# Kernel tuning notes

Hardware: AMD Instinct MI355X
Metric: run time of the kernel (lower is better)

## Reference

```python
import jax, jax.numpy as jnp
import numpy as np
import math

CODE_DIMS = [32, 32]
NUM_CODEBOOK = 16
FEAT_DIM = 1024
EPS = 1e-12


def rms_norm(x, eps=EPS):
    var = jnp.mean(x * x, axis=-1, keepdims=True) + eps
    return x * jax.lax.rsqrt(var)


def outer_product(y, code_dims):
    # y: [..., h, sum(code_dims)] -> [..., h, prod(code_dims)]
    splits = list(np.cumsum(code_dims)[:-1])
    mats = jnp.split(y, splits, axis=-1)
    out = mats[0]
    for m in mats[1:]:
        out = out[..., :, None] * m[..., None, :]
        out = out.reshape(*out.shape[:-2], -1)
    return out


def setup_inputs() -> dict:
    key = jax.random.key(0)
    kx, kw = jax.random.split(key)
    x = jax.random.normal(kx, (4, 2048, FEAT_DIM), dtype=jnp.float32)
    std = math.sqrt(2.0 / (FEAT_DIM + sum(CODE_DIMS)))
    weight = jax.random.normal(kw, (NUM_CODEBOOK, FEAT_DIM, sum(CODE_DIMS)), dtype=jnp.float32) * std
    return {"x": x, "weight": weight}


def reference(x, weight):
    h = weight.shape[0]
    # batched per-codebook linear: [..., d] x [h, d, o] -> [..., h, o]
    y = jnp.einsum('...i,hio->...ho', x, weight)
    # chunked outer product per codebook -> [..., h, prod(code_dims)]
    op = outer_product(y, CODE_DIMS)
    out = jnp.mean(op, axis=-2) * math.sqrt(h)
    return rms_norm(out)
```

## Files before the change

kernel.cpp:

```cpp
#include <hip/hip_runtime.h>
#include <hip/hip_bf16.h>

#define KDIM  1024
#define NOUT  1024
#define NTOK  8192
#define NCB   16
#define BM    256
#define BN    128
#define BK    64
#define TILEB 49152
#define NBUF  3

typedef __attribute__((ext_vector_type(8))) short short8;
typedef __attribute__((ext_vector_type(4))) float f32x4;

__device__ static inline unsigned short f2bf(float f) {
    unsigned int u = __float_as_uint(f);
    return (unsigned short)((u + 0x7FFFu + ((u >> 16) & 1u)) >> 16);
}

__device__ static inline float bf2f(unsigned int h) {
    return __uint_as_float(h << 16);
}

__device__ static inline void async_copy16(const void* g, void* l) {
    __builtin_amdgcn_global_load_lds(
        (const __attribute__((address_space(1))) void*)g,
        (__attribute__((address_space(3))) void*)l, 16, 0, 0);
}

__global__ __launch_bounds__(256) void conv_kernel(const float* __restrict__ x,
                                                   const float* __restrict__ W,
                                                   unsigned short* __restrict__ A,
                                                   unsigned short* __restrict__ Bt) {
    int b = blockIdx.x;
    if (b < 4096) {
        int u = b * 256 + threadIdx.x;
        const float* src = x + (size_t)u * 8;
        float4 v0 = *(const float4*)(src);
        float4 v1 = *(const float4*)(src + 4);
        short8 o;
        o[0] = (short)f2bf(v0.x); o[1] = (short)f2bf(v0.y);
        o[2] = (short)f2bf(v0.z); o[3] = (short)f2bf(v0.w);
        o[4] = (short)f2bf(v1.x); o[5] = (short)f2bf(v1.y);
        o[6] = (short)f2bf(v1.z); o[7] = (short)f2bf(v1.w);
        *(short8*)(A + (size_t)u * 8) = o;
    } else {
        int u = (b - 4096) * 256 + threadIdx.x;
        int n  = u & (NOUT - 1);
        int k0 = (u >> 10) << 3;
        int h = n >> 6, o = n & 63;
        const float* src = W + (size_t)h * KDIM * 64 + o;
        short8 v;
#pragma unroll
        for (int j = 0; j < 8; ++j)
            v[j] = (short)f2bf(src[(size_t)(k0 + j) * 64]);
        *(short8*)(Bt + (size_t)n * KDIM + k0) = v;
    }
}


template <int VM, bool STAGE>
__device__ __forceinline__ void phase0(const unsigned short* __restrict__ A,
                                       const unsigned short* __restrict__ Bt,
                                       char* lds, int tid, int m0, int n0, int kt,
                                       int wm, int wn, int r15, int q,
                                       f32x4 (&acc)[4][4]) {
    asm volatile("s_waitcnt vmcnt(%0)" :: "i"(VM) : "memory");
    __builtin_amdgcn_sched_barrier(0);
    __builtin_amdgcn_s_barrier();
    __builtin_amdgcn_sched_barrier(0);
    if (STAGE) {
        char* lb = lds + ((kt + 2) % NBUF) * TILEB;
        unsigned short* Als = (unsigned short*)lb;
        unsigned short* Bls = (unsigned short*)(lb + 32768);
        const int kel = (kt + 2) * BK;
#pragma unroll
        for (int i = 0; i < 2; ++i) {
            int s = i * 512 + tid;
            int row = s >> 3;
            int cs = (s & 7) ^ (row & 7);
            async_copy16(A + (size_t)(m0 + row) * KDIM + kel + cs * 8, Als + s * 8);
        }
        {
            int s = tid;
            int row = s >> 3;
            int cs = (s & 7) ^ (row & 7);
            async_copy16(Bt + (size_t)(n0 + row) * KDIM + kel + cs * 8, Bls + s * 8);
        }
    }
    const unsigned short* Al = (const unsigned short*)(lds + (kt % NBUF) * TILEB);
    const unsigned short* Bl = Al + 16384;
    short8 af[4], bf[4];
#pragma unroll
    for (int mf = 0; mf < 4; ++mf) {
        int row = wm * 64 + mf * 16 + r15;
        af[mf] = *(const short8*)(Al + row * 64 + ((q ^ (row & 7)) << 3));
    }
#pragma unroll
    for (int nf = 0; nf < 4; ++nf) {
        int row = wn * 64 + nf * 16 + r15;
        bf[nf] = *(const short8*)(Bl + row * 64 + ((q ^ (row & 7)) << 3));
    }
    asm volatile("s_waitcnt lgkmcnt(0)" ::: "memory");
    __builtin_amdgcn_sched_barrier(0);
    __builtin_amdgcn_s_setprio(1);
#pragma unroll
    for (int mf = 0; mf < 4; ++mf)
#pragma unroll
        for (int nf = 0; nf < 4; ++nf)
            acc[mf][nf] = __builtin_amdgcn_mfma_f32_16x16x32_bf16(af[mf], bf[nf], acc[mf][nf], 0, 0, 0);
    __builtin_amdgcn_s_setprio(0);
}

template <bool STAGE>
__device__ __forceinline__ void phase1(const unsigned short* __restrict__ A,
                                       const unsigned short* __restrict__ Bt,
                                       char* lds, int tid, int m0, int n0, int kt,
                                       int wm, int wn, int r15, int q,
                                       f32x4 (&acc)[4][4]) {
    __builtin_amdgcn_s_barrier();
    __builtin_amdgcn_sched_barrier(0);
    if (STAGE) {
        char* lb = lds + ((kt + 2) % NBUF) * TILEB;
        unsigned short* Als = (unsigned short*)lb;
        unsigned short* Bls = (unsigned short*)(lb + 32768);
        const int kel = (kt + 2) * BK;
#pragma unroll
        for (int i = 2; i < 4; ++i) {
            int s = i * 512 + tid;
            int row = s >> 3;
            int cs = (s & 7) ^ (row & 7);
            async_copy16(A + (size_t)(m0 + row) * KDIM + kel + cs * 8, Als + s * 8);
        }
        {
            int s = 512 + tid;
            int row = s >> 3;
            int cs = (s & 7) ^ (row & 7);
            async_copy16(Bt + (size_t)(n0 + row) * KDIM + kel + cs * 8, Bls + s * 8);
        }
    }
    const unsigned short* Al = (const unsigned short*)(lds + (kt % NBUF) * TILEB);
    const unsigned short* Bl = Al + 16384;
    short8 af[4], bf[4];
#pragma unroll
    for (int mf = 0; mf < 4; ++mf) {
        int row = wm * 64 + mf * 16 + r15;
        af[mf] = *(const short8*)(Al + row * 64 + (((4 + q) ^ (row & 7)) << 3));
    }
#pragma unroll
    for (int nf = 0; nf < 4; ++nf) {
        int row = wn * 64 + nf * 16 + r15;
        bf[nf] = *(const short8*)(Bl + row * 64 + (((4 + q) ^ (row & 7)) << 3));
    }
    asm volatile("s_waitcnt lgkmcnt(0)" ::: "memory");
    __builtin_amdgcn_sched_barrier(0);
    __builtin_amdgcn_s_setprio(1);
#pragma unroll
    for (int mf = 0; mf < 4; ++mf)
#pragma unroll
        for (int nf = 0; nf < 4; ++nf)
            acc[mf][nf] = __builtin_amdgcn_mfma_f32_16x16x32_bf16(af[mf], bf[nf], acc[mf][nf], 0, 0, 0);
    __builtin_amdgcn_s_setprio(0);
}

__device__ __forceinline__ void stage_full(const unsigned short* __restrict__ A,
                                           const unsigned short* __restrict__ Bt,
                                           char* lbase, int tid, int m0, int n0, int kel) {
    unsigned short* Als = (unsigned short*)lbase;
    unsigned short* Bls = (unsigned short*)(lbase + 32768);
#pragma unroll
    for (int i = 0; i < 4; ++i) {
        int s = i * 512 + tid;
        int row = s >> 3;
        int cs = (s & 7) ^ (row & 7);
        async_copy16(A + (size_t)(m0 + row) * KDIM + kel + cs * 8, Als + s * 8);
    }
#pragma unroll
    for (int i = 0; i < 2; ++i) {
        int s = i * 512 + tid;
        int row = s >> 3;
        int cs = (s & 7) ^ (row & 7);
        async_copy16(Bt + (size_t)(n0 + row) * KDIM + kel + cs * 8, Bls + s * 8);
    }
}

__global__ __launch_bounds__(512, 2) void gemm_kernel(const unsigned short* __restrict__ A,
                                                      const unsigned short* __restrict__ Bt,
                                                      unsigned short* __restrict__ Y) {
    extern __shared__ char lds[];

    const int id  = blockIdx.x;
    const int xcd = id & 7;
    const int j   = id >> 3;
    const int m0  = (xcd * 4 + (j >> 3)) * BM;
    const int n0  = (j & 7) * BN;

    const int tid  = threadIdx.x;
    const int lane = tid & 63;
    const int w    = tid >> 6;
    const int wm   = w >> 1;
    const int wn   = w & 1;
    const int r15  = lane & 15;
    const int q    = lane >> 4;

    f32x4 acc[4][4];
#pragma unroll
    for (int mf = 0; mf < 4; ++mf)
#pragma unroll
        for (int nf = 0; nf < 4; ++nf)
            acc[mf][nf] = (f32x4){0.f, 0.f, 0.f, 0.f};

    stage_full(A, Bt, lds,         tid, m0, n0, 0);
    stage_full(A, Bt, lds + TILEB, tid, m0, n0, BK);

#pragma unroll 1
    for (int kt = 0; kt < 14; ++kt) {
        phase0<6, true>(A, Bt, lds, tid, m0, n0, kt, wm, wn, r15, q, acc);
        phase1<true>   (A, Bt, lds, tid, m0, n0, kt, wm, wn, r15, q, acc);
    }
    phase0<6, false>(A, Bt, lds, tid, m0, n0, 14, wm, wn, r15, q, acc);
    phase1<false>   (A, Bt, lds, tid, m0, n0, 14, wm, wn, r15, q, acc);
    phase0<0, false>(A, Bt, lds, tid, m0, n0, 15, wm, wn, r15, q, acc);
    phase1<false>   (A, Bt, lds, tid, m0, n0, 15, wm, wn, r15, q, acc);

#pragma unroll
    for (int mf = 0; mf < 4; ++mf)
#pragma unroll
        for (int nf = 0; nf < 4; ++nf) {
            int col = n0 + wn * 64 + nf * 16 + r15;
#pragma unroll
            for (int r = 0; r < 4; ++r) {
                int row = m0 + wm * 64 + mf * 16 + q * 4 + r;
                Y[(size_t)row * NOUT + col] = f2bf(acc[mf][nf][r]);
            }
        }
}

__global__ __launch_bounds__(256) void epilogue_kernel(const unsigned short* __restrict__ Y,
                                                       float* __restrict__ out) {
    __shared__ float ylds[1024];
    __shared__ float red[4];

    const int t = blockIdx.x;
    const int tid = threadIdx.x;
    const unsigned short* yrow = Y + (size_t)t * NOUT;

    {
        uint2 raw = *(const uint2*)(yrow + tid * 4);
        ylds[tid * 4 + 0] = bf2f(raw.x & 0xffffu);
        ylds[tid * 4 + 1] = bf2f(raw.x >> 16);
        ylds[tid * 4 + 2] = bf2f(raw.y & 0xffffu);
        ylds[tid * 4 + 3] = bf2f(raw.y >> 16);
    }
    __syncthreads();

    const int jj = tid >> 3;
    const int k0 = (tid & 7) * 4;

    float o0 = 0.f, o1 = 0.f, o2 = 0.f, o3 = 0.f;
#pragma unroll
    for (int h = 0; h < NCB; ++h) {
        float a = ylds[h * 64 + jj];
        float4 bb = *(const float4*)&ylds[h * 64 + 32 + k0];
        o0 += a * bb.x; o1 += a * bb.y; o2 += a * bb.z; o3 += a * bb.w;
    }
    o0 *= 0.25f; o1 *= 0.25f; o2 *= 0.25f; o3 *= 0.25f;

    float ss = o0 * o0 + o1 * o1 + o2 * o2 + o3 * o3;
#pragma unroll
    for (int off = 32; off >= 1; off >>= 1)
        ss += __shfl_xor(ss, off, 64);

    const int lane = tid & 63, wv = tid >> 6;
    if (lane == 0) red[wv] = ss;
    __syncthreads();
    float tot = red[0] + red[1] + red[2] + red[3];
    float scale = rsqrtf(tot * (1.0f / 1024.0f) + 1e-12f);

    float4 o;
    o.x = o0 * scale; o.y = o1 * scale; o.z = o2 * scale; o.w = o3 * scale;
    *(float4*)(out + (size_t)t * 1024 + tid * 4) = o;
}

extern "C" void kernel_launch(void* const* d_in, const int* in_sizes, int n_in,
                              void* d_out, int out_size, void* d_ws, size_t ws_size,
                              hipStream_t stream) {
    const float* x   = (const float*)d_in[0];
    const float* wgt = (const float*)d_in[1];
    float* out = (float*)d_out;

    unsigned short* A  = (unsigned short*)d_ws;
    unsigned short* Bt = (unsigned short*)((char*)d_ws + (16u << 20));
    unsigned short* Y  = (unsigned short*)((char*)d_ws + (18u << 20));

    (void)hipFuncSetAttribute((const void*)gemm_kernel,
                              hipFuncAttributeMaxDynamicSharedMemorySize, NBUF * TILEB);

    conv_kernel<<<4096 + 512, 256, 0, stream>>>(x, wgt, A, Bt);
    gemm_kernel<<<(NTOK / BM) * (NOUT / BN), 512, NBUF * TILEB, stream>>>(A, Bt, Y);
    epilogue_kernel<<<NTOK, 256, 0, stream>>>(Y, out);
}
```

Baseline: 48.40 us.

## Double-buffer MFMA register fragments and remap blocks to XCDs in conv/epilogue

The GEMM main loop now prefetches the next half-tile's A/B fragments from LDS into a second register set while MFMAs run on the current set, with partial lgkmcnt waits replacing full drains. Global-to-LDS staging is split into halves, with a vmcnt wait per phase. The conversion and epilogue kernels also remap block indices so each XCD handles a contiguous range of rows. This is meant to hide LDS read latency behind matrix math and improve L2 locality, at the cost of more VGPRs and more delicate waitcnt accounting.

```diff
diff --git a/kernel.cpp b/kernel.cpp
--- a/kernel.cpp
+++ b/kernel.cpp
@@ -35,7 +35,8 @@
                                                    unsigned short* __restrict__ Bt) {
     int b = blockIdx.x;
     if (b < 4096) {
-        int u = b * 256 + threadIdx.x;
+        int bb = (b & 7) * 512 + (b >> 3);
+        int u = bb * 256 + threadIdx.x;
         const float* src = x + (size_t)u * 8;
         float4 v0 = *(const float4*)(src);
         float4 v1 = *(const float4*)(src + 4);
@@ -60,129 +61,96 @@
 }
 
 
+__device__ __forceinline__ void stage_half(const unsigned short* __restrict__ A,
+                                           const unsigned short* __restrict__ Bt,
+                                           char* lbase, int tid, int m0, int n0,
+                                           int kel, int half) {
+    unsigned short* Als = (unsigned short*)lbase;
+    unsigned short* Bls = (unsigned short*)(lbase + 32768);
+#pragma unroll
+    for (int i = 0; i < 2; ++i) {
+        int s = (half * 2 + i) * 512 + tid;
+        int row = s >> 3;
+        int cs = (s & 7) ^ (row & 7);
+        async_copy16(A + (size_t)(m0 + row) * KDIM + kel + cs * 8, Als + s * 8);
+    }
+    {
+        int s = half * 512 + tid;
+        int row = s >> 3;
+        int cs = (s & 7) ^ (row & 7);
+        async_copy16(Bt + (size_t)(n0 + row) * KDIM + kel + cs * 8, Bls + s * 8);
+    }
+}
+
+__device__ __forceinline__ void read_frags(const char* lds, int buf, int chunk,
+                                           int wm, int wn, int r15, int q,
+                                           short8 (&af)[4], short8 (&bf)[4]) {
+    const unsigned short* Al = (const unsigned short*)(lds + buf * TILEB);
+    const unsigned short* Bl = Al + 16384;
+#pragma unroll
+    for (int mf = 0; mf < 4; ++mf) {
+        int row = wm * 64 + mf * 16 + r15;
+        af[mf] = *(const short8*)(Al + row * 64 + (((chunk + q) ^ (row & 7)) << 3));
+    }
+#pragma unroll
+    for (int nf = 0; nf < 4; ++nf) {
+        int row = wn * 64 + nf * 16 + r15;
+        bf[nf] = *(const short8*)(Bl + row * 64 + (((chunk + q) ^ (row & 7)) << 3));
+    }
+}
+
+__device__ __forceinline__ void mfma16(short8 (&af)[4], short8 (&bf)[4], f32x4 (&acc)[4][4]) {
+    __builtin_amdgcn_s_setprio(1);
+#pragma unroll
+    for (int mf = 0; mf < 4; ++mf)
+#pragma unroll
+        for (int nf = 0; nf < 4; ++nf)
+            acc[mf][nf] = __builtin_amdgcn_mfma_f32_16x16x32_bf16(af[mf], bf[nf], acc[mf][nf], 0, 0, 0);
+    __builtin_amdgcn_s_setprio(0);
+}
+
 template <int VM, bool STAGE>
 __device__ __forceinline__ void phase0(const unsigned short* __restrict__ A,
                                        const unsigned short* __restrict__ Bt,
                                        char* lds, int tid, int m0, int n0, int kt,
                                        int wm, int wn, int r15, int q,
+                                       short8 (&afc)[4], short8 (&bfc)[4],
+                                       short8 (&afn)[4], short8 (&bfn)[4],
                                        f32x4 (&acc)[4][4]) {
     asm volatile("s_waitcnt vmcnt(%0)" :: "i"(VM) : "memory");
     __builtin_amdgcn_sched_barrier(0);
     __builtin_amdgcn_s_barrier();
     __builtin_amdgcn_sched_barrier(0);
-    if (STAGE) {
-        char* lb = lds + ((kt + 2) % NBUF) * TILEB;
-        unsigned short* Als = (unsigned short*)lb;
-        unsigned short* Bls = (unsigned short*)(lb + 32768);
-        const int kel = (kt + 2) * BK;
-#pragma unroll
-        for (int i = 0; i < 2; ++i) {
-            int s = i * 512 + tid;
-            int row = s >> 3;
-            int cs = (s & 7) ^ (row & 7);
-            async_copy16(A + (size_t)(m0 + row) * KDIM + kel + cs * 8, Als + s * 8);
-        }
-        {
-            int s = tid;
-            int row = s >> 3;
-            int cs = (s & 7) ^ (row & 7);
-            async_copy16(Bt + (size_t)(n0 + row) * KDIM + kel + cs * 8, Bls + s * 8);
-        }
-    }
-    const unsigned short* Al = (const unsigned short*)(lds + (kt % NBUF) * TILEB);
-    const unsigned short* Bl = Al + 16384;
-    short8 af[4], bf[4];
-#pragma unroll
-    for (int mf = 0; mf < 4; ++mf) {
-        int row = wm * 64 + mf * 16 + r15;
-        af[mf] = *(const short8*)(Al + row * 64 + ((q ^ (row & 7)) << 3));
-    }
-#pragma unroll
-    for (int nf = 0; nf < 4; ++nf) {
-        int row = wn * 64 + nf * 16 + r15;
-        bf[nf] = *(const short8*)(Bl + row * 64 + ((q ^ (row & 7)) << 3));
-    }
-    asm volatile("s_waitcnt lgkmcnt(0)" ::: "memory");
-    __builtin_amdgcn_sched_barrier(0);
-    __builtin_amdgcn_s_setprio(1);
-#pragma unroll
-    for (int mf = 0; mf < 4; ++mf)
-#pragma unroll
-        for (int nf = 0; nf < 4; ++nf)
-            acc[mf][nf] = __builtin_amdgcn_mfma_f32_16x16x32_bf16(af[mf], bf[nf], acc[mf][nf], 0, 0, 0);
-    __builtin_amdgcn_s_setprio(0);
-}
-
-template <bool STAGE>
+    if (STAGE)
+        stage_half(A, Bt, lds + ((kt + 2) % NBUF) * TILEB, tid, m0, n0, (kt + 2) * BK, 0);
+    read_frags(lds, kt % NBUF, 4, wm, wn, r15, q, afn, bfn);
+    asm volatile("s_waitcnt lgkmcnt(8)" ::: "memory");
+    __builtin_amdgcn_sched_barrier(0);
+    mfma16(afc, bfc, acc);
+}
+
+template <int VM, bool STAGE, bool PRE>
 __device__ __forceinline__ void phase1(const unsigned short* __restrict__ A,
                                        const unsigned short* __restrict__ Bt,
                                        char* lds, int tid, int m0, int n0, int kt,
                                        int wm, int wn, int r15, int q,
+                                       short8 (&afc)[4], short8 (&bfc)[4],
+                                       short8 (&afn)[4], short8 (&bfn)[4],
                                        f32x4 (&acc)[4][4]) {
+    asm volatile("s_waitcnt vmcnt(%0)" :: "i"(VM) : "memory");
+    __builtin_amdgcn_sched_barrier(0);
     __builtin_amdgcn_s_barrier();
     __builtin_amdgcn_sched_barrier(0);
-    if (STAGE) {
-        char* lb = lds + ((kt + 2) % NBUF) * TILEB;
-        unsigned short* Als = (unsigned short*)lb;
-        unsigned short* Bls = (unsigned short*)(lb + 32768);
-        const int kel = (kt + 2) * BK;
-#pragma unroll
-        for (int i = 2; i < 4; ++i) {
-            int s = i * 512 + tid;
-            int row = s >> 3;
-            int cs = (s & 7) ^ (row & 7);
-            async_copy16(A + (size_t)(m0 + row) * KDIM + kel + cs * 8, Als + s * 8);
-        }
-        {
-            int s = 512 + tid;
-            int row = s >> 3;
-            int cs = (s & 7) ^ (row & 7);
-            async_copy16(Bt + (size_t)(n0 + row) * KDIM + kel + cs * 8, Bls + s * 8);
-        }
-    }
-    const unsigned short* Al = (const unsigned short*)(lds + (kt % NBUF) * TILEB);
-    const unsigned short* Bl = Al + 16384;
-    short8 af[4], bf[4];
-#pragma unroll
-    for (int mf = 0; mf < 4; ++mf) {
-        int row = wm * 64 + mf * 16 + r15;
-        af[mf] = *(const short8*)(Al + row * 64 + (((4 + q) ^ (row & 7)) << 3));
-    }
-#pragma unroll
-    for (int nf = 0; nf < 4; ++nf) {
-        int row = wn * 64 + nf * 16 + r15;
-        bf[nf] = *(const short8*)(Bl + row * 64 + (((4 + q) ^ (row & 7)) << 3));
-    }
-    asm volatile("s_waitcnt lgkmcnt(0)" ::: "memory");
-    __builtin_amdgcn_sched_barrier(0);
-    __builtin_amdgcn_s_setprio(1);
-#pragma unroll
-    for (int mf = 0; mf < 4; ++mf)
-#pragma unroll
-        for (int nf = 0; nf < 4; ++nf)
-            acc[mf][nf] = __builtin_amdgcn_mfma_f32_16x16x32_bf16(af[mf], bf[nf], acc[mf][nf], 0, 0, 0);
-    __builtin_amdgcn_s_setprio(0);
-}
-
-__device__ __forceinline__ void stage_full(const unsigned short* __restrict__ A,
-                                           const unsigned short* __restrict__ Bt,
-                                           char* lbase, int tid, int m0, int n0, int kel) {
-    unsigned short* Als = (unsigned short*)lbase;
-    unsigned short* Bls = (unsigned short*)(lbase + 32768);
-#pragma unroll
-    for (int i = 0; i < 4; ++i) {
-        int s = i * 512 + tid;
-        int row = s >> 3;
-        int cs = (s & 7) ^ (row & 7);
-        async_copy16(A + (size_t)(m0 + row) * KDIM + kel + cs * 8, Als + s * 8);
-    }
-#pragma unroll
-    for (int i = 0; i < 2; ++i) {
-        int s = i * 512 + tid;
-        int row = s >> 3;
-        int cs = (s & 7) ^ (row & 7);
-        async_copy16(Bt + (size_t)(n0 + row) * KDIM + kel + cs * 8, Bls + s * 8);
-    }
+    if (STAGE)
+        stage_half(A, Bt, lds + ((kt + 2) % NBUF) * TILEB, tid, m0, n0, (kt + 2) * BK, 1);
+    if (PRE) {
+        read_frags(lds, (kt + 1) % NBUF, 0, wm, wn, r15, q, afn, bfn);
+        asm volatile("s_waitcnt lgkmcnt(8)" ::: "memory");
+    } else {
+        asm volatile("s_waitcnt lgkmcnt(0)" ::: "memory");
+    }
+    __builtin_amdgcn_sched_barrier(0);
+    mfma16(afc, bfc, acc);
 }
 
 __global__ __launch_bounds__(512, 2) void gemm_kernel(const unsigned short* __restrict__ A,
@@ -211,18 +179,26 @@
         for (int nf = 0; nf < 4; ++nf)
             acc[mf][nf] = (f32x4){0.f, 0.f, 0.f, 0.f};
 
-    stage_full(A, Bt, lds,         tid, m0, n0, 0);
-    stage_full(A, Bt, lds + TILEB, tid, m0, n0, BK);
+    short8 aF0[4], bF0[4], aF1[4], bF1[4];
+
+    stage_half(A, Bt, lds,         tid, m0, n0, 0,  0);
+    stage_half(A, Bt, lds,         tid, m0, n0, 0,  1);
+    stage_half(A, Bt, lds + TILEB, tid, m0, n0, BK, 0);
+    stage_half(A, Bt, lds + TILEB, tid, m0, n0, BK, 1);
+    asm volatile("s_waitcnt vmcnt(6)" ::: "memory");
+    __builtin_amdgcn_sched_barrier(0);
+    __builtin_amdgcn_s_barrier();
+    read_frags(lds, 0, 0, wm, wn, r15, q, aF0, bF0);
 
 #pragma unroll 1
     for (int kt = 0; kt < 14; ++kt) {
-        phase0<6, true>(A, Bt, lds, tid, m0, n0, kt, wm, wn, r15, q, acc);
-        phase1<true>   (A, Bt, lds, tid, m0, n0, kt, wm, wn, r15, q, acc);
-    }
-    phase0<6, false>(A, Bt, lds, tid, m0, n0, 14, wm, wn, r15, q, acc);
-    phase1<false>   (A, Bt, lds, tid, m0, n0, 14, wm, wn, r15, q, acc);
-    phase0<0, false>(A, Bt, lds, tid, m0, n0, 15, wm, wn, r15, q, acc);
-    phase1<false>   (A, Bt, lds, tid, m0, n0, 15, wm, wn, r15, q, acc);
+        phase0<6, true>   (A, Bt, lds, tid, m0, n0, kt, wm, wn, r15, q, aF0, bF0, aF1, bF1, acc);
+        phase1<3, true, true>(A, Bt, lds, tid, m0, n0, kt, wm, wn, r15, q, aF1, bF1, aF0, bF0, acc);
+    }
+    phase0<6, false>       (A, Bt, lds, tid, m0, n0, 14, wm, wn, r15, q, aF0, bF0, aF1, bF1, acc);
+    phase1<0, false, true> (A, Bt, lds, tid, m0, n0, 14, wm, wn, r15, q, aF1, bF1, aF0, bF0, acc);
+    phase0<0, false>       (A, Bt, lds, tid, m0, n0, 15, wm, wn, r15, q, aF0, bF0, aF1, bF1, acc);
+    phase1<0, false, false>(A, Bt, lds, tid, m0, n0, 15, wm, wn, r15, q, aF1, bF1, aF0, bF0, acc);
 
 #pragma unroll
     for (int mf = 0; mf < 4; ++mf)
@@ -242,7 +218,7 @@
     __shared__ float ylds[1024];
     __shared__ float red[4];
 
-    const int t = blockIdx.x;
+    const int t = (blockIdx.x & 7) * 1024 + (blockIdx.x >> 3);
     const int tid = threadIdx.x;
     const unsigned short* yrow = Y + (size_t)t * NOUT;
 
```

Result: no change. 47.59 us (-1.7%).
